# Kernel tuning notes

Hardware: AMD Instinct MI355X
Metric: run time of the kernel (lower is better)

The kernel has to match this reference:

```python
import jax, jax.numpy as jnp
import numpy as np

E = 576        # embed_dims
HEADS = 18
NPTS = 12
NF = 3         # num_frames
DD = 2 * NF - 1  # depth of value volume (5)
HD = E // HEADS  # head dim (32)


def _grid_init_bias():
    # Faithful reproduction of init_weights() for sampling_offsets.bias
    theta = np.arange(8) * (2.0 * np.pi / 8)
    yaw = np.stack([np.cos(theta), np.sin(theta), np.zeros(8)], -1)
    roll = np.stack([np.zeros(8), np.cos(theta), np.sin(theta)], -1)
    pitch = np.stack([np.cos(theta), np.zeros(8), np.sin(theta)], -1)
    g = np.concatenate([yaw, pitch[[1, 2, 3, 5, 6, 7]], roll[[1, 3, 5, 7]]], 0)  # (18,3)
    g = g / np.abs(g).max(-1, keepdims=True)
    g = np.tile(g[:, None, None, :], (1, 1, NPTS, 1))              # (18,1,12,3)
    g = g * np.arange(1, NPTS + 1, dtype=np.float64)[None, None, :, None]
    return g.reshape(-1).astype(np.float32)                        # (18*12*3,)


def setup_inputs() -> dict:
    key = jax.random.key(0)
    ks = jax.random.split(key, 6)
    bs, h, w = 2, 64, 80
    nq = h * w
    lim = float(np.sqrt(6.0 / (E + E)))  # xavier uniform for square E x E
    return {
        "query": jax.random.normal(ks[0], (bs, nq, E), jnp.float32),
        "value": jax.random.normal(ks[1], (bs, nq * DD, E), jnp.float32),
        "query_pos": jax.random.normal(ks[2], (bs, nq, E), jnp.float32),
        "W_off": jnp.zeros((E, HEADS * NPTS * 3), jnp.float32),  # constant_init 0
        "b_off": jnp.asarray(_grid_init_bias()),
        "W_attn": jnp.zeros((E, HEADS * NPTS), jnp.float32),
        "b_attn": jnp.zeros((HEADS * NPTS,), jnp.float32),
        "W_v": jax.random.uniform(ks[3], (E, E), jnp.float32, -lim, lim),
        "b_v": jnp.zeros((E,), jnp.float32),
        "W_out": jax.random.uniform(ks[4], (E, E), jnp.float32, -lim, lim),
        "b_out": jnp.zeros((E,), jnp.float32),
        "h": 64,
        "w": 80,
    }


def _deform_attn_3d(value, loc, attn, D, H, W):
    # value: (bs, D*H*W, heads, hd)  token order: depth-major (D, H, W)
    # loc:   (bs, nq, heads, np, 3)  normalized (x, y, z) in [0,1]
    # attn:  (bs, nq, heads, np)
    bs, _, heads, hd = value.shape
    nq = loc.shape[1]
    # (bs, heads, D*H*W, hd) flat spatial for gathers
    v = value.reshape(bs, D, H, W, heads, hd).transpose(0, 4, 1, 2, 3, 5)
    v = v.reshape(bs, heads, D * H * W, hd)
    lt = jnp.moveaxis(loc, 2, 1)    # (bs, heads, nq, np, 3)
    at = jnp.moveaxis(attn, 2, 1)   # (bs, heads, nq, np)
    # grid_sample(align_corners=False) coordinate convention: pix = u*size - 0.5
    x = lt[..., 0] * W - 0.5
    y = lt[..., 1] * H - 0.5
    z = lt[..., 2] * D - 0.5
    x0 = jnp.floor(x); y0 = jnp.floor(y); z0 = jnp.floor(z)
    fx = x - x0; fy = y - y0; fz = z - z0
    acc = jnp.zeros((bs, heads, nq, NPTS, hd), v.dtype)
    for dz in (0, 1):
        for dy in (0, 1):
            for dx in (0, 1):
                xi = x0 + dx; yi = y0 + dy; zi = z0 + dz
                wgt = ((fx if dx else 1.0 - fx)
                       * (fy if dy else 1.0 - fy)
                       * (fz if dz else 1.0 - fz))
                valid = ((xi >= 0) & (xi < W) & (yi >= 0) & (yi < H)
                         & (zi >= 0) & (zi < D))
                xc = jnp.clip(xi, 0, W - 1).astype(jnp.int32)
                yc = jnp.clip(yi, 0, H - 1).astype(jnp.int32)
                zc = jnp.clip(zi, 0, D - 1).astype(jnp.int32)
                idx = ((zc * H + yc) * W + xc).reshape(bs, heads, nq * NPTS)
                g = jnp.take_along_axis(v, idx[..., None], axis=2)
                g = g.reshape(bs, heads, nq, NPTS, hd)
                acc = acc + g * (wgt * valid.astype(v.dtype))[..., None]
    out = jnp.einsum("bhqp,bhqpd->bhqd", at, acc)  # softmax-weighted sum over points
    return out.transpose(0, 2, 1, 3).reshape(bs, nq, heads * hd)


def _forward(query, value, query_pos, W_off, b_off, W_attn, b_attn,
             W_v, b_v, W_out, b_out, h, w):
    bs, nq, _ = query.shape
    q = query + query_pos
    v = (value @ W_v + b_v).reshape(bs, nq * DD, HEADS, HD)
    offs = (q @ W_off + b_off).reshape(bs, nq, HEADS, NPTS, 3)
    attn = jax.nn.softmax((q @ W_attn + b_attn).reshape(bs, nq, HEADS, NPTS), axis=-1)
    # reference points: pixel centers normalized, z = 0
    ry, rx = jnp.meshgrid((jnp.arange(h, dtype=jnp.float32) + 0.5) / h,
                          (jnp.arange(w, dtype=jnp.float32) + 0.5) / w,
                          indexing="ij")
    ref = jnp.stack([rx.reshape(-1), ry.reshape(-1),
                     jnp.zeros(h * w, jnp.float32)], -1)  # (nq, 3)
    norm = jnp.array([w, h, NF], jnp.float32)  # NOTE: z normalized by num_frames (as in source)
    loc = ref[None, :, None, None, :] + offs / norm
    out = _deform_attn_3d(v, loc, attn, DD, h, w)
    return out @ W_out + b_out  # dropout is identity at eval


def reference(query, value, query_pos, W_off, b_off, W_attn, b_attn,
              W_v, b_v, W_out, b_out, h, w):
    return _forward(query, value, query_pos, W_off, b_off, W_attn, b_attn,
                    W_v, b_v, W_out, b_out, h, w)
```

## Files before the change

kernel.cpp:

```cpp
#include <hip/hip_runtime.h>
#include <cstdint>

#define E_DIM   576
#define HEADS   18
#define NPTS    12
#define DDEPTH  5
#define HDIM    32
#define BSZ     2
#define GH      64
#define GW      80
#define NQ      (GH*GW)
#define NTOK    (NQ*DDEPTH)
#define MIXW    864
#define BQ_TOT  (BSZ*NQ)

typedef __attribute__((ext_vector_type(8))) short short8;
typedef __attribute__((ext_vector_type(4))) float f32x4;
typedef __attribute__((ext_vector_type(4))) uint32_t u32x4;

__device__ __forceinline__ float b2f_lo(uint32_t u) {
    union { uint32_t u; float f; } v; v.u = u << 16; return v.f;
}
__device__ __forceinline__ float b2f_hi(uint32_t u) {
    union { uint32_t u; float f; } v; v.u = u & 0xffff0000u; return v.f;
}
__device__ __forceinline__ ushort f2b(float f) {
    union { float f; uint32_t u; } v; v.f = f;
    return (ushort)((v.u + 0x7fffu + ((v.u >> 16) & 1u)) >> 16);
}

__global__ void prep_weights(const float* __restrict__ W_v, const float* __restrict__ W_out,
                             const float* __restrict__ W_off, const float* __restrict__ W_attn,
                             const float* __restrict__ b_off, const float* __restrict__ b_attn,
                             ushort* __restrict__ wt_v, ushort* __restrict__ wt_out,
                             ushort* __restrict__ wt_mix, float* __restrict__ bias_mix) {
    int idx = blockIdx.x * blockDim.x + threadIdx.x;
    if (idx < 864) bias_mix[idx] = (idx < 648) ? b_off[idx] : b_attn[idx - 648];
    if (idx < 331776) {
        int n = idx / E_DIM, k = idx - n * E_DIM;
        wt_v[idx] = f2b(W_v[(size_t)k * E_DIM + n]);
    } else if (idx < 663552) {
        int j = idx - 331776;
        int n = j / E_DIM, k = j - n * E_DIM;
        wt_out[j] = f2b(W_out[(size_t)k * E_DIM + n]);
    } else if (idx < 1161216) {
        int j = idx - 663552;
        int n = j / E_DIM, k = j - n * E_DIM;
        float v = (n < 648) ? W_off[(size_t)k * 648 + n] : W_attn[(size_t)k * 216 + (n - 648)];
        wt_mix[j] = f2b(v);
    }
}

#define TM 128
#define TN 96
#define BK 32

#define AM_BF16   0
#define AM_F32    1
#define AM_F32ADD 2

__device__ __forceinline__ void async_cp16(const ushort* gsrc, ushort* ldst) {
    __builtin_amdgcn_global_load_lds(
        (const __attribute__((address_space(1))) void*)gsrc,
        (__attribute__((address_space(3))) void*)ldst, 16, 0, 0);
}

__device__ __forceinline__ void xcd_map(int id, int total, int nbn, int& bx, int& by) {
    const int xcd = id & 7;
    const int pos = id >> 3;
    const int logical = xcd * (total >> 3) + pos;
    by = logical % nbn;
    bx = logical / nbn;
}

template <int AMODE, typename OutT>
__device__ __forceinline__ void gemm_body(ushort* __restrict__ smem, int bx, int by,
                                          const void* __restrict__ Apv,
                                          const float* __restrict__ A2,
                                          const ushort* __restrict__ Bt,
                                          const float* __restrict__ bias,
                                          OutT* __restrict__ C, int K, int ldc) {
    ushort* Asb = smem;
    ushort* Bsb = smem + TM * BK;
    const int tid  = threadIdx.x;
    const int wave = tid >> 6;
    const int lane = tid & 63;
    const int m16  = lane & 15;
    const int quad = lane >> 4;
    const int wr   = wave >> 1;
    const int wc   = wave & 1;
    const int row0 = bx * TM;
    const int n0   = by * TN;

    const f32x4 zero = {0.f, 0.f, 0.f, 0.f};
    f32x4 acc[4][3];
    #pragma unroll
    for (int rt = 0; rt < 4; ++rt)
        #pragma unroll
        for (int ct = 0; ct < 3; ++ct) acc[rt][ct] = zero;

    const int srow = lane >> 2;
    const int scol = (((lane & 3) ^ ((lane >> 3) & 3))) * 8;
    const int ksw  = (quad ^ ((m16 >> 1) & 3)) * 8;

    const int srow_f = ((wave & 1) << 6) | lane;
    const int khalf  = wave >> 1;
    const float* A32  = (const float*)Apv;
    const ushort* A16 = (const ushort*)Apv;
    const float* arow  = A32 + (size_t)(row0 + srow_f) * K + khalf * 16;
    const float* arow2 = (AMODE == AM_F32ADD)
                         ? A2 + (size_t)(row0 + srow_f) * K + khalf * 16 : nullptr;

    for (int k0 = 0; k0 < K; k0 += BK) {
        float4 av0, av1, av2, av3, bv0, bv1, bv2, bv3;
        if constexpr (AMODE == AM_BF16) {
            #pragma unroll
            for (int c = 0; c < 2; ++c) {
                const int ch = wave + c * 4;
                async_cp16(A16 + (size_t)(row0 + ch * 16 + srow) * K + k0 + scol,
                           Asb + ch * 512 + lane * 8);
            }
        } else {
            av0 = *reinterpret_cast<const float4*>(arow + k0);
            av1 = *reinterpret_cast<const float4*>(arow + k0 + 4);
            av2 = *reinterpret_cast<const float4*>(arow + k0 + 8);
            av3 = *reinterpret_cast<const float4*>(arow + k0 + 12);
            if constexpr (AMODE == AM_F32ADD) {
                bv0 = *reinterpret_cast<const float4*>(arow2 + k0);
                bv1 = *reinterpret_cast<const float4*>(arow2 + k0 + 4);
                bv2 = *reinterpret_cast<const float4*>(arow2 + k0 + 8);
                bv3 = *reinterpret_cast<const float4*>(arow2 + k0 + 12);
            }
        }
        async_cp16(Bt + (size_t)(n0 + wave * 16 + srow) * K + k0 + scol,
                   Bsb + wave * 512 + lane * 8);
        if (wave < 2)
            async_cp16(Bt + (size_t)(n0 + (wave + 4) * 16 + srow) * K + k0 + scol,
                       Bsb + (wave + 4) * 512 + lane * 8);

        if constexpr (AMODE != AM_BF16) {
            if constexpr (AMODE == AM_F32ADD) {
                av0.x += bv0.x; av0.y += bv0.y; av0.z += bv0.z; av0.w += bv0.w;
                av1.x += bv1.x; av1.y += bv1.y; av1.z += bv1.z; av1.w += bv1.w;
                av2.x += bv2.x; av2.y += bv2.y; av2.z += bv2.z; av2.w += bv2.w;
                av3.x += bv3.x; av3.y += bv3.y; av3.z += bv3.z; av3.w += bv3.w;
            }
            const int r  = srow_f & 15;
            const int ck = srow_f >> 4;
            const int xr = (r >> 1) & 3;
            const int s0 = khalf * 2;
            u32x4 w0 = {(uint32_t)f2b(av0.x) | ((uint32_t)f2b(av0.y) << 16),
                        (uint32_t)f2b(av0.z) | ((uint32_t)f2b(av0.w) << 16),
                        (uint32_t)f2b(av1.x) | ((uint32_t)f2b(av1.y) << 16),
                        (uint32_t)f2b(av1.z) | ((uint32_t)f2b(av1.w) << 16)};
            u32x4 w1 = {(uint32_t)f2b(av2.x) | ((uint32_t)f2b(av2.y) << 16),
                        (uint32_t)f2b(av2.z) | ((uint32_t)f2b(av2.w) << 16),
                        (uint32_t)f2b(av3.x) | ((uint32_t)f2b(av3.y) << 16),
                        (uint32_t)f2b(av3.z) | ((uint32_t)f2b(av3.w) << 16)};
            *reinterpret_cast<u32x4*>(&Asb[ck * 512 + r * 32 + ((s0 ^ xr) * 8)]) = w0;
            *reinterpret_cast<u32x4*>(&Asb[ck * 512 + r * 32 + (((s0 + 1) ^ xr) * 8)]) = w1;
        }
        __syncthreads();

        short8 afrag[4], bfrag[3];
        #pragma unroll
        for (int rt = 0; rt < 4; ++rt)
            afrag[rt] = *reinterpret_cast<const short8*>(
                Asb + (wr * 4 + rt) * 512 + m16 * 32 + ksw);
        #pragma unroll
        for (int ct = 0; ct < 3; ++ct)
            bfrag[ct] = *reinterpret_cast<const short8*>(
                Bsb + (wc * 3 + ct) * 512 + m16 * 32 + ksw);

        #pragma unroll
        for (int rt = 0; rt < 4; ++rt)
            #pragma unroll
            for (int ct = 0; ct < 3; ++ct)
                acc[rt][ct] = __builtin_amdgcn_mfma_f32_16x16x32_bf16(
                    afrag[rt], bfrag[ct], acc[rt][ct], 0, 0, 0);

        __syncthreads();
    }

    #pragma unroll
    for (int ct = 0; ct < 3; ++ct) {
        const int col = n0 + wc * 48 + ct * 16 + m16;
        const float bcol = bias[col];
        #pragma unroll
        for (int rt = 0; rt < 4; ++rt) {
            #pragma unroll
            for (int r = 0; r < 4; ++r) {
                const int row = row0 + wr * 64 + rt * 16 + quad * 4 + r;
                const float val = acc[rt][ct][r] + bcol;
                if constexpr (__is_same(OutT, float)) {
                    C[(size_t)row * ldc + col] = val;
                } else {
                    C[(size_t)row * ldc + col] = f2b(val);
                }
            }
        }
    }
}

__global__ void gemm_out(const ushort* __restrict__ A, const ushort* __restrict__ Bt,
                         const float* __restrict__ bias, float* __restrict__ C,
                         int K, int ldc, int total, int nbn) {
    __shared__ __align__(16) ushort smem[(TM + TN) * BK];
    int bx, by;
    xcd_map(blockIdx.x, total, nbn, bx, by);
    gemm_body<AM_BF16, float>(smem, bx, by, A, nullptr, Bt, bias, C, K, ldc);
}

__global__ void gemm_dual(const float* __restrict__ q, const float* __restrict__ qp,
                          const ushort* __restrict__ B1,
                          const float* __restrict__ bias1, float* __restrict__ C1,
                          int K1, int ldc1, int nbn1, int split,
                          const float* __restrict__ val, const ushort* __restrict__ B2,
                          const float* __restrict__ bias2, ushort* __restrict__ C2,
                          int K2, int ldc2, int nbn2, int total2) {
    __shared__ __align__(16) ushort smem[(TM + TN) * BK];
    const int id = blockIdx.x;
    int bx, by;
    if (id < split) {
        xcd_map(id, split, nbn1, bx, by);
        gemm_body<AM_F32ADD, float>(smem, bx, by, q, qp, B1, bias1, C1, K1, ldc1);
    } else {
        xcd_map(id - split, total2, nbn2, bx, by);
        gemm_body<AM_F32, ushort>(smem, bx, by, val, nullptr, B2, bias2, C2, K2, ldc2);
    }
}

__global__ void __launch_bounds__(256, 8)
deform_kernel(const ushort* __restrict__ vbuf,
              const float* __restrict__ mix,
              ushort* __restrict__ aout) {
    __shared__ uint2 corn[16 * 97];
    __shared__ int   ccnt[16];
    const int gl   = threadIdx.x >> 4;
    const int l    = threadIdx.x & 15;
    const int head = blockIdx.x / 640;
    const int bq   = (blockIdx.x % 640) * 16 + gl;
    const int q    = bq % NQ;
    const int b    = bq / NQ;
    const int qx   = q % GW;
    const int qy   = q / GW;

    const float* mrow = mix + (size_t)bq * MIXW;

    float lg = (l < NPTS) ? mrow[648 + head * NPTS + l] : -1e30f;
    float mx = lg;
    #pragma unroll
    for (int mk = 1; mk < 16; mk <<= 1) mx = fmaxf(mx, __shfl_xor(mx, mk, 16));
    float e = (l < NPTS) ? __expf(lg - mx) : 0.f;
    float s = e;
    #pragma unroll
    for (int mk = 1; mk < 16; mk <<= 1) s += __shfl_xor(s, mk, 16);

    float    cw[8];
    uint32_t coff[8];
    uint32_t mask = 0;
    {
        const float ap = e / s;
        const int pl = (l < NPTS) ? l : 0;
        const int ob = (head * NPTS + pl) * 3;
        const float ox = mrow[ob + 0];
        const float oy = mrow[ob + 1];
        const float oz = mrow[ob + 2];
        const float x = (float)qx + ox;
        const float y = (float)qy + oy;
        const float z = oz * (5.0f / 3.0f) - 0.5f;
        const float x0f = floorf(x), y0f = floorf(y), z0f = floorf(z);
        const int x0 = (int)x0f, y0 = (int)y0f, z0 = (int)z0f;
        const float fx = x - x0f, fy = y - y0f, fz = z - z0f;

        #pragma unroll
        for (int dz = 0; dz < 2; ++dz) {
            const int zi = z0 + dz;
            const bool zv = (zi >= 0) & (zi < DDEPTH);
            const int zc = min(max(zi, 0), DDEPTH - 1);
            const float wz = dz ? fz : 1.f - fz;
            #pragma unroll
            for (int dy = 0; dy < 2; ++dy) {
                const int yi = y0 + dy;
                const bool yv = (yi >= 0) & (yi < GH);
                const int yc = min(max(yi, 0), GH - 1);
                const float wy = dy ? fy : 1.f - fy;
                #pragma unroll
                for (int dx = 0; dx < 2; ++dx) {
                    const int xi = x0 + dx;
                    const bool xv = (xi >= 0) & (xi < GW);
                    const int xc = min(max(xi, 0), GW - 1);
                    const float wx = dx ? fx : 1.f - fx;
                    const int i = dz * 4 + dy * 2 + dx;
                    const bool valid = zv & yv & xv & (l < NPTS);
                    cw[i]   = ap * wz * wy * wx;
                    coff[i] = (uint32_t)((zc * GH + yc) * GW + xc) * (E_DIM / 2);
                    mask |= (valid ? (1u << i) : 0u);
                }
            }
        }
    }

    const int cnt = __popc(mask);
    int pre = cnt;
    #pragma unroll
    for (int mk = 1; mk < 16; mk <<= 1) {
        const int t = __shfl_up(pre, mk, 16);
        if (l >= mk) pre += t;
    }
    int o = gl * 97 + (pre - cnt);
    #pragma unroll
    for (int i = 0; i < 8; ++i) {
        if (mask & (1u << i)) {
            uint2 w; w.x = __float_as_uint(cw[i]); w.y = coff[i];
            corn[o] = w;
            ++o;
        }
    }
    if (l == 15) ccnt[gl] = pre;
    __syncthreads();

    const uint32_t lbase = (uint32_t)b * (uint32_t)(NTOK * (E_DIM / 2))
                         + (uint32_t)(head * (HDIM / 2) + l);
    const uint32_t* vb32 = reinterpret_cast<const uint32_t*>(vbuf);
    const int n = ccnt[gl];
    const uint2* cg = &corn[gl * 97];
    float o0 = 0.f, o1 = 0.f;
    #pragma unroll 2
    for (int j = 0; j < n; ++j) {
        const uint2 wo = cg[j];
        const uint32_t pair = vb32[lbase + wo.y];
        const float w = __uint_as_float(wo.x);
        o0 += w * b2f_lo(pair);
        o1 += w * b2f_hi(pair);
    }
    const uint32_t packed = (uint32_t)f2b(o0) | ((uint32_t)f2b(o1) << 16);
    reinterpret_cast<uint32_t*>(aout)[(size_t)bq * (E_DIM / 2) + head * (HDIM / 2) + l] = packed;
}

extern "C" void kernel_launch(void* const* d_in, const int* in_sizes, int n_in,
                              void* d_out, int out_size, void* d_ws, size_t ws_size,
                              hipStream_t stream) {
    const float* query     = (const float*)d_in[0];
    const float* value     = (const float*)d_in[1];
    const float* query_pos = (const float*)d_in[2];
    const float* W_off     = (const float*)d_in[3];
    const float* b_off     = (const float*)d_in[4];
    const float* W_attn    = (const float*)d_in[5];
    const float* b_attn    = (const float*)d_in[6];
    const float* W_v       = (const float*)d_in[7];
    const float* b_v       = (const float*)d_in[8];
    const float* W_out     = (const float*)d_in[9];
    const float* b_out     = (const float*)d_in[10];
    float* out = (float*)d_out;

    char* ws = (char*)d_ws;
    ushort* vbuf     = (ushort*)(ws);
    ushort* aout     = (ushort*)(ws + 58982400);
    float*  mixb     = (float*) (ws + 70778880);
    ushort* wt_v     = (ushort*)(ws + 106168320);
    ushort* wt_out   = (ushort*)(ws + 106831872);
    ushort* wt_mix   = (ushort*)(ws + 107495424);
    float*  bias_mix = (float*) (ws + 108490752);

    prep_weights<<<(1161216 + 255) / 256, 256, 0, stream>>>(
        W_v, W_out, W_off, W_attn, b_off, b_attn, wt_v, wt_out, wt_mix, bias_mix);

    gemm_dual<<<720 + 2400, 256, 0, stream>>>(
        query, query_pos, wt_mix, bias_mix, mixb, E_DIM, MIXW, 9, 720,
        value, wt_v, b_v, vbuf, E_DIM, E_DIM, 6, 2400);

    deform_kernel<<<HEADS * 640, 256, 0, stream>>>(vbuf, mixb, aout);

    gemm_out<<<480, 256, 0, stream>>>(
        aout, wt_out, b_out, out, E_DIM, E_DIM, 480, 6);
}
```

Before: 433.5 us.

## Double-buffer shared memory in fp32-input GEMM path to overlap loads with MFMA

For the fp32-input GEMM modes used by gemm_dual, the code now keeps two shared-memory buffers for the A and B tiles. The next k-tile's global loads and async copies are issued before the current tile's MFMAs, and the converted A data is written afterwards, leaving one barrier per iteration instead of two. This aims to hide global-load latency behind compute. It doubles LDS use per block, which may reduce occupancy, and raises register pressure from holding the prefetched values.

```diff
diff --git a/kernel.cpp b/kernel.cpp
--- a/kernel.cpp
+++ b/kernel.cpp
@@ -80,8 +80,6 @@
                                           const ushort* __restrict__ Bt,
                                           const float* __restrict__ bias,
                                           OutT* __restrict__ C, int K, int ldc) {
-    ushort* Asb = smem;
-    ushort* Bsb = smem + TM * BK;
     const int tid  = threadIdx.x;
     const int wave = tid >> 6;
     const int lane = tid & 63;
@@ -103,24 +101,61 @@
     const int scol = (((lane & 3) ^ ((lane >> 3) & 3))) * 8;
     const int ksw  = (quad ^ ((m16 >> 1) & 3)) * 8;
 
-    const int srow_f = ((wave & 1) << 6) | lane;
-    const int khalf  = wave >> 1;
-    const float* A32  = (const float*)Apv;
-    const ushort* A16 = (const ushort*)Apv;
-    const float* arow  = A32 + (size_t)(row0 + srow_f) * K + khalf * 16;
-    const float* arow2 = (AMODE == AM_F32ADD)
-                         ? A2 + (size_t)(row0 + srow_f) * K + khalf * 16 : nullptr;
-
-    for (int k0 = 0; k0 < K; k0 += BK) {
-        float4 av0, av1, av2, av3, bv0, bv1, bv2, bv3;
-        if constexpr (AMODE == AM_BF16) {
+    auto readfrag_mfma = [&](ushort* Asb, ushort* Bsb) {
+        short8 afrag[4], bfrag[3];
+        #pragma unroll
+        for (int rt = 0; rt < 4; ++rt)
+            afrag[rt] = *reinterpret_cast<const short8*>(
+                Asb + (wr * 4 + rt) * 512 + m16 * 32 + ksw);
+        #pragma unroll
+        for (int ct = 0; ct < 3; ++ct)
+            bfrag[ct] = *reinterpret_cast<const short8*>(
+                Bsb + (wc * 3 + ct) * 512 + m16 * 32 + ksw);
+        #pragma unroll
+        for (int rt = 0; rt < 4; ++rt)
+            #pragma unroll
+            for (int ct = 0; ct < 3; ++ct)
+                acc[rt][ct] = __builtin_amdgcn_mfma_f32_16x16x32_bf16(
+                    afrag[rt], bfrag[ct], acc[rt][ct], 0, 0, 0);
+    };
+    auto stageB = [&](ushort* Bsb, int k0) {
+        async_cp16(Bt + (size_t)(n0 + wave * 16 + srow) * K + k0 + scol,
+                   Bsb + wave * 512 + lane * 8);
+        if (wave < 2)
+            async_cp16(Bt + (size_t)(n0 + (wave + 4) * 16 + srow) * K + k0 + scol,
+                       Bsb + (wave + 4) * 512 + lane * 8);
+    };
+
+    if constexpr (AMODE == AM_BF16) {
+        ushort* Asb = smem;
+        ushort* Bsb = smem + TM * BK;
+        const ushort* A16 = (const ushort*)Apv;
+        for (int k0 = 0; k0 < K; k0 += BK) {
             #pragma unroll
             for (int c = 0; c < 2; ++c) {
                 const int ch = wave + c * 4;
                 async_cp16(A16 + (size_t)(row0 + ch * 16 + srow) * K + k0 + scol,
                            Asb + ch * 512 + lane * 8);
             }
-        } else {
+            stageB(Bsb, k0);
+            __syncthreads();
+            readfrag_mfma(Asb, Bsb);
+            __syncthreads();
+        }
+    } else {
+        ushort* Asb0 = smem;
+        ushort* Bsb0 = smem + TM * BK;
+        ushort* Asb1 = smem + (TM + TN) * BK;
+        ushort* Bsb1 = Asb1 + TM * BK;
+
+        const int srow_f = ((wave & 1) << 6) | lane;
+        const int khalf  = wave >> 1;
+        const float* arow  = (const float*)Apv + (size_t)(row0 + srow_f) * K + khalf * 16;
+        const float* arow2 = (AMODE == AM_F32ADD)
+                             ? A2 + (size_t)(row0 + srow_f) * K + khalf * 16 : nullptr;
+
+        float4 av0, av1, av2, av3, bv0, bv1, bv2, bv3;
+        auto issueA = [&](int k0) {
             av0 = *reinterpret_cast<const float4*>(arow + k0);
             av1 = *reinterpret_cast<const float4*>(arow + k0 + 4);
             av2 = *reinterpret_cast<const float4*>(arow + k0 + 8);
@@ -131,14 +166,8 @@
                 bv2 = *reinterpret_cast<const float4*>(arow2 + k0 + 8);
                 bv3 = *reinterpret_cast<const float4*>(arow2 + k0 + 12);
             }
-        }
-        async_cp16(Bt + (size_t)(n0 + wave * 16 + srow) * K + k0 + scol,
-                   Bsb + wave * 512 + lane * 8);
-        if (wave < 2)
-            async_cp16(Bt + (size_t)(n0 + (wave + 4) * 16 + srow) * K + k0 + scol,
-                       Bsb + (wave + 4) * 512 + lane * 8);
-
-        if constexpr (AMODE != AM_BF16) {
+        };
+        auto writeA = [&](ushort* Asb) {
             if constexpr (AMODE == AM_F32ADD) {
                 av0.x += bv0.x; av0.y += bv0.y; av0.z += bv0.z; av0.w += bv0.w;
                 av1.x += bv1.x; av1.y += bv1.y; av1.z += bv1.z; av1.w += bv1.w;
@@ -159,27 +188,29 @@
                         (uint32_t)f2b(av3.z) | ((uint32_t)f2b(av3.w) << 16)};
             *reinterpret_cast<u32x4*>(&Asb[ck * 512 + r * 32 + ((s0 ^ xr) * 8)]) = w0;
             *reinterpret_cast<u32x4*>(&Asb[ck * 512 + r * 32 + (((s0 + 1) ^ xr) * 8)]) = w1;
+        };
+
+        issueA(0);
+        stageB(Bsb0, 0);
+        writeA(Asb0);
+        __syncthreads();
+
+        int cur = 0;
+        for (int k0 = 0; k0 < K; k0 += BK) {
+            ushort* Acur = cur ? Asb1 : Asb0;
+            ushort* Bcur = cur ? Bsb1 : Bsb0;
+            ushort* Anxt = cur ? Asb0 : Asb1;
+            ushort* Bnxt = cur ? Bsb0 : Bsb1;
+            const bool nx = (k0 + BK < K);
+            if (nx) {
+                issueA(k0 + BK);
+                stageB(Bnxt, k0 + BK);
+            }
+            readfrag_mfma(Acur, Bcur);
+            if (nx) writeA(Anxt);
+            __syncthreads();
+            cur ^= 1;
         }
-        __syncthreads();
-
-        short8 afrag[4], bfrag[3];
-        #pragma unroll
-        for (int rt = 0; rt < 4; ++rt)
-            afrag[rt] = *reinterpret_cast<const short8*>(
-                Asb + (wr * 4 + rt) * 512 + m16 * 32 + ksw);
-        #pragma unroll
-        for (int ct = 0; ct < 3; ++ct)
-            bfrag[ct] = *reinterpret_cast<const short8*>(
-                Bsb + (wc * 3 + ct) * 512 + m16 * 32 + ksw);
-
-        #pragma unroll
-        for (int rt = 0; rt < 4; ++rt)
-            #pragma unroll
-            for (int ct = 0; ct < 3; ++ct)
-                acc[rt][ct] = __builtin_amdgcn_mfma_f32_16x16x32_bf16(
-                    afrag[rt], bfrag[ct], acc[rt][ct], 0, 0, 0);
-
-        __syncthreads();
     }
 
     #pragma unroll
@@ -218,7 +249,7 @@
                           const float* __restrict__ val, const ushort* __restrict__ B2,
                           const float* __restrict__ bias2, ushort* __restrict__ C2,
                           int K2, int ldc2, int nbn2, int total2) {
-    __shared__ __align__(16) ushort smem[(TM + TN) * BK];
+    __shared__ __align__(16) ushort smem[2 * (TM + TN) * BK];
     const int id = blockIdx.x;
     int bx, by;
     if (id < split) {
```

Measured after the change: 432.0 us. No clear change (-0.3%).
